# Kernel optimization log

Hardware: AMD Instinct MI355X
Metric: run time of the kernel (lower is better)

## Reference

```python
import jax, jax.numpy as jnp
import numpy as np

N, E, T = 20000, 320000, 4
F_IN, HID, F_OUT = 128, 256, 128
EPS = 1e-5  # torch BatchNorm1d default


def _gcn_layer(x, src, dst, ew, W, b, gamma, beta):
    # gather-scale-scatter: out[dst] += ew_e * x[src]
    msgs = ew[:, :, None] * x[src]                      # (E, T, F)
    agg = jax.ops.segment_sum(msgs, dst, num_segments=N)  # (N, T, F)
    h = jnp.einsum('ntf,fh->nth', agg, W) + b            # (N, T, H)
    # BatchNorm1d over channel dim H (training-mode batch stats over N and T)
    mean = h.mean(axis=(0, 1))
    var = h.var(axis=(0, 1))
    h = (h - mean) * jax.lax.rsqrt(var + EPS) * gamma + beta
    return jax.nn.relu(h)


def setup_inputs() -> dict:
    key = jax.random.key(0)
    ks = jax.random.split(key, 8)
    node_features = jax.random.normal(ks[0], (N, T, F_IN), jnp.float32)
    edge_index = jax.random.randint(ks[1], (2, E), 0, N, dtype=jnp.int32)
    edges_weight = jax.random.uniform(ks[2], (E, T), jnp.float32)
    s0 = 1.0 / np.sqrt(F_IN)
    s1 = 1.0 / np.sqrt(HID)
    W0 = jax.random.uniform(ks[3], (F_IN, HID), jnp.float32, -s0, s0)
    b0 = jax.random.uniform(ks[4], (HID,), jnp.float32, -s0, s0)
    W1 = jax.random.uniform(ks[5], (HID, F_OUT), jnp.float32, -s1, s1)
    b1 = jax.random.uniform(ks[6], (F_OUT,), jnp.float32, -s1, s1)
    g0 = jnp.ones((HID,), jnp.float32)
    be0 = jnp.zeros((HID,), jnp.float32)
    g1 = jnp.ones((F_OUT,), jnp.float32)
    be1 = jnp.zeros((F_OUT,), jnp.float32)
    return {"node_features": node_features, "edge_index": edge_index,
            "edges_weight": edges_weight, "W0": W0, "b0": b0, "g0": g0,
            "be0": be0, "W1": W1, "b1": b1, "g1": g1, "be1": be1}


def reference(node_features, edge_index, edges_weight,
              W0, b0, g0, be0, W1, b1, g1, be1):
    src, dst = edge_index[0], edge_index[1]
    h = _gcn_layer(node_features, src, dst, edges_weight, W0, b0, g0, be0)
    h = _gcn_layer(h, src, dst, edges_weight, W1, b1, g1, be1)
    return h
```

## Files before the change

### kernel.cpp

```cpp
#include <hip/hip_runtime.h>


#define T_DIM 4
#define F_DIM 128
#define HID   256
#define TF    512

__global__ void count_kernel(const int* __restrict__ dst, int E, int* __restrict__ deg) {
    int e = blockIdx.x * blockDim.x + threadIdx.x;
    if (e < E) atomicAdd(&deg[dst[e]], 1);
}

__global__ void scan_kernel(const int* __restrict__ deg, int* __restrict__ row_start,
                            int* __restrict__ cursor, int n) {
    __shared__ int part[1024];
    int tid = threadIdx.x;
    int chunk = (n + 1023) >> 10;
    int begin = tid * chunk;
    if (begin > n) begin = n;
    int end = begin + chunk;
    if (end > n) end = n;
    int s = 0;
    for (int i = begin; i < end; ++i) s += deg[i];
    part[tid] = s;
    __syncthreads();
    for (int off = 1; off < 1024; off <<= 1) {
        int v = (tid >= off) ? part[tid - off] : 0;
        __syncthreads();
        part[tid] += v;
        __syncthreads();
    }
    int excl = (tid == 0) ? 0 : part[tid - 1];
    for (int i = begin; i < end; ++i) {
        row_start[i] = excl;
        cursor[i] = excl;
        excl += deg[i];
    }
    if (tid == 1023) row_start[n] = part[1023];
}

__global__ void fill_kernel(const int* __restrict__ src, const int* __restrict__ dst,
                            const float4* __restrict__ ew, int E,
                            int* __restrict__ cursor, int* __restrict__ esrc,
                            float4* __restrict__ ewr) {
    int e = blockIdx.x * blockDim.x + threadIdx.x;
    if (e < E) {
        int d = dst[e];
        int p = atomicAdd(&cursor[d], 1);
        esrc[p] = src[e];
        ewr[p] = ew[e];
    }
}

__global__ __launch_bounds__(256) void agg_kernel(
        const float* __restrict__ x, const float* __restrict__ ewr,
        const int* __restrict__ row_start, const int* __restrict__ esrc,
        float* __restrict__ out) {
    const int n = blockIdx.x;
    const int j = threadIdx.x;
    const int t0 = j >> 7;
    const int beg = row_start[n], end = row_start[n + 1];
    float acc0 = 0.f, acc1 = 0.f;
    for (int i = beg; i < end; ++i) {
        const int s = esrc[i];
        const float* xr = x + (size_t)s * TF;
        const float w0 = ewr[i * T_DIM + t0];
        const float w1 = ewr[i * T_DIM + t0 + 2];
        acc0 = fmaf(w0, xr[j], acc0);
        acc1 = fmaf(w1, xr[j + 256], acc1);
    }
    const size_t o = (size_t)n * TF + j;
    out[o] = acc0;
    out[o + 256] = acc1;
}

template<int K, int NC, bool FUSE>
__global__ __launch_bounds__(256, 4) void gemm_kernel(
        const float* __restrict__ A, const float* __restrict__ W,
        const float* __restrict__ scale, const float* __restrict__ shift,
        float* __restrict__ out) {
    constexpr int BM = 128, BN = 128, BK = 32;
    constexpr int ASTR = BK + 4;
    __shared__ float Al[BM * ASTR];
    __shared__ float Wl[BK * BN];
    const int tid = threadIdx.x;
    const long rowbase = (long)blockIdx.y * BM;
    const int colbase = blockIdx.x * BN;
    const int trow = tid >> 4;
    const int tcol = tid & 15;

    float acc[8][8] = {};

    const int nk = K / BK;
    for (int kb = 0; kb < nk; ++kb) {
        #pragma unroll
        for (int it = 0; it < 4; ++it) {
            int idx = tid + it * 256;
            int r = idx >> 3, q = idx & 7;
            float4 v = *(const float4*)&A[(rowbase + r) * K + kb * BK + q * 4];
            if (FUSE) {
                int ch = kb * BK + q * 4;
                float4 sc = *(const float4*)&scale[ch];
                float4 sh = *(const float4*)&shift[ch];
                v.x = fmaxf(fmaf(sc.x, v.x, sh.x), 0.f);
                v.y = fmaxf(fmaf(sc.y, v.y, sh.y), 0.f);
                v.z = fmaxf(fmaf(sc.z, v.z, sh.z), 0.f);
                v.w = fmaxf(fmaf(sc.w, v.w, sh.w), 0.f);
            }
            *(float4*)&Al[r * ASTR + q * 4] = v;
        }
        #pragma unroll
        for (int it = 0; it < 4; ++it) {
            int idx = tid + it * 256;
            int k = idx >> 5, c4 = idx & 31;
            *(float4*)&Wl[k * BN + c4 * 4] =
                *(const float4*)&W[(long)(kb * BK + k) * NC + colbase + c4 * 4];
        }
        __syncthreads();

        #pragma unroll
        for (int kk = 0; kk < BK; ++kk) {
            float a[8], w[8];
            #pragma unroll
            for (int i = 0; i < 8; ++i) a[i] = Al[(trow + 16 * i) * ASTR + kk];
            *(float4*)&w[0] = *(const float4*)&Wl[kk * BN + tcol * 8];
            *(float4*)&w[4] = *(const float4*)&Wl[kk * BN + tcol * 8 + 4];
            #pragma unroll
            for (int i = 0; i < 8; ++i)
                #pragma unroll
                for (int j = 0; j < 8; ++j)
                    acc[i][j] = fmaf(a[i], w[j], acc[i][j]);
        }
        __syncthreads();
    }

    #pragma unroll
    for (int i = 0; i < 8; ++i) {
        float* op = &out[(rowbase + trow + 16 * i) * NC + colbase + tcol * 8];
        *(float4*)&op[0] = make_float4(acc[i][0], acc[i][1], acc[i][2], acc[i][3]);
        *(float4*)&op[4] = make_float4(acc[i][4], acc[i][5], acc[i][6], acc[i][7]);
    }
}

template<int C>
__global__ __launch_bounds__(256) void stats_kernel(
        const float* __restrict__ h, int rows,
        float* __restrict__ sums, float* __restrict__ sqs) {
    constexpr int Q = C / 4;
    constexpr int RPB = 256 / Q;
    const int q = threadIdx.x & (Q - 1);
    const int sub = threadIdx.x / Q;
    float4 s = make_float4(0.f, 0.f, 0.f, 0.f);
    float4 s2 = make_float4(0.f, 0.f, 0.f, 0.f);
    for (long r = (long)blockIdx.x * RPB + sub; r < rows; r += (long)gridDim.x * RPB) {
        float4 v = *(const float4*)&h[r * C + q * 4];
        s.x += v.x; s.y += v.y; s.z += v.z; s.w += v.w;
        s2.x = fmaf(v.x, v.x, s2.x); s2.y = fmaf(v.y, v.y, s2.y);
        s2.z = fmaf(v.z, v.z, s2.z); s2.w = fmaf(v.w, v.w, s2.w);
    }
    __shared__ float4 redS[256], redQ[256];
    redS[threadIdx.x] = s;
    redQ[threadIdx.x] = s2;
    __syncthreads();
    if (sub == 0) {
        #pragma unroll
        for (int u = 1; u < RPB; ++u) {
            float4 a = redS[u * Q + q], b = redQ[u * Q + q];
            s.x += a.x; s.y += a.y; s.z += a.z; s.w += a.w;
            s2.x += b.x; s2.y += b.y; s2.z += b.z; s2.w += b.w;
        }
        atomicAdd(&sums[q * 4 + 0], s.x);
        atomicAdd(&sums[q * 4 + 1], s.y);
        atomicAdd(&sums[q * 4 + 2], s.z);
        atomicAdd(&sums[q * 4 + 3], s.w);
        atomicAdd(&sqs[q * 4 + 0], s2.x);
        atomicAdd(&sqs[q * 4 + 1], s2.y);
        atomicAdd(&sqs[q * 4 + 2], s2.z);
        atomicAdd(&sqs[q * 4 + 3], s2.w);
    }
}

__global__ void finalize_kernel(const float* __restrict__ sums, const float* __restrict__ sqs,
                                const float* __restrict__ g, const float* __restrict__ be,
                                float* __restrict__ scale, float* __restrict__ shift,
                                int C, float invR) {
    int c = threadIdx.x;
    if (c < C) {
        float mean = sums[c] * invR;
        float var = sqs[c] * invR - mean * mean;
        float a = g[c] * rsqrtf(var + 1e-5f);
        scale[c] = a;
        shift[c] = fmaf(-mean, a, be[c]);
    }
}

__global__ void bnapply_kernel(const float4* __restrict__ h4,
                               const float* __restrict__ scale, const float* __restrict__ shift,
                               float4* __restrict__ out4, int n4) {
    int i = blockIdx.x * 256 + threadIdx.x;
    if (i >= n4) return;
    float4 v = h4[i];
    int cb = (i & 31) << 2;
    float4 sc = *(const float4*)&scale[cb];
    float4 sh = *(const float4*)&shift[cb];
    v.x = fmaxf(fmaf(sc.x, v.x, sh.x), 0.f);
    v.y = fmaxf(fmaf(sc.y, v.y, sh.y), 0.f);
    v.z = fmaxf(fmaf(sc.z, v.z, sh.z), 0.f);
    v.w = fmaxf(fmaf(sc.w, v.w, sh.w), 0.f);
    out4[i] = v;
}

extern "C" void kernel_launch(void* const* d_in, const int* in_sizes, int n_in,
                              void* d_out, int out_size, void* d_ws, size_t ws_size,
                              hipStream_t stream) {
    const float* x   = (const float*)d_in[0];
    const int*   ei  = (const int*)d_in[1];
    const float* ew  = (const float*)d_in[2];
    const float* W0  = (const float*)d_in[3];
    const float* g0  = (const float*)d_in[5];
    const float* be0 = (const float*)d_in[6];
    const float* W1  = (const float*)d_in[7];
    const float* g1  = (const float*)d_in[9];
    const float* be1 = (const float*)d_in[10];
    float* out = (float*)d_out;

    const int N = in_sizes[0] / TF;
    const int E = in_sizes[1] / 2;
    const int ROWS = N * T_DIM;

    const int* src = ei;
    const int* dst = ei + E;

    float* h1   = (float*)d_ws;
    float* bufC = h1 + (size_t)ROWS * HID;
    float* h2   = bufC + (size_t)ROWS * F_DIM;
    int* deg       = (int*)(h2 + (size_t)ROWS * F_DIM);
    int* row_start = deg + N;
    int* cursor    = row_start + N + 1;
    int* esrc      = cursor + N + 1;
    float* ewr     = (float*)(esrc + E);
    float* sums0   = ewr + (size_t)E * 4;
    float* sqs0    = sums0 + HID;
    float* sums1   = sqs0 + HID;
    float* sqs1    = sums1 + F_DIM;
    float* scale0  = sqs1 + F_DIM;
    float* shift0  = scale0 + HID;
    float* scale1  = shift0 + HID;
    float* shift1  = scale1 + F_DIM;

    hipMemsetAsync(deg, 0, N * sizeof(int), stream);
    hipMemsetAsync(sums0, 0, (2 * HID + 2 * F_DIM) * sizeof(float), stream);

    const int eb = (E + 255) / 256;
    count_kernel<<<eb, 256, 0, stream>>>(dst, E, deg);
    scan_kernel<<<1, 1024, 0, stream>>>(deg, row_start, cursor, N);
    fill_kernel<<<eb, 256, 0, stream>>>(src, dst, (const float4*)ew, E, cursor,
                                        esrc, (float4*)ewr);

    agg_kernel<<<N, 256, 0, stream>>>(x, ewr, row_start, esrc, bufC);
    gemm_kernel<128, 256, false><<<dim3(2, ROWS / 128), 256, 0, stream>>>(
        bufC, W0, nullptr, nullptr, h1);
    stats_kernel<256><<<256, 256, 0, stream>>>(h1, ROWS, sums0, sqs0);
    finalize_kernel<<<1, 256, 0, stream>>>(sums0, sqs0, g0, be0, scale0, shift0, HID,
                                           1.f / (float)ROWS);

    gemm_kernel<256, 128, true><<<dim3(1, ROWS / 128), 256, 0, stream>>>(
        h1, W1, scale0, shift0, bufC);
    agg_kernel<<<N, 256, 0, stream>>>(bufC, ewr, row_start, esrc, h2);
    stats_kernel<128><<<256, 256, 0, stream>>>(h2, ROWS, sums1, sqs1);
    finalize_kernel<<<1, 128, 0, stream>>>(sums1, sqs1, g1, be1, scale1, shift1, F_DIM,
                                           1.f / (float)ROWS);
    bnapply_kernel<<<(ROWS * F_DIM / 4 + 255) / 256, 256, 0, stream>>>(
        (const float4*)h2, scale1, shift1, (float4*)out, ROWS * F_DIM / 4);
}
```

Before: 651.3 us.

## Split aggregation edges across thread groups and vectorize GEMM shared-memory reads

The aggregation kernel now has four 64-thread groups, each handling every fourth edge with float4 loads of 8 features per thread. The per-group partial sums are then reduced through shared memory, so more gather loads are in flight per node. The GEMM reads A as float4 across four k-steps and uses a strided column mapping for W reads and output stores, which is meant to cut shared-memory bank conflicts. The second GEMM uses a 64-row tile to launch more blocks. The trade-offs are the extra shared-memory reduction and sync in aggregation, and idle groups on low-degree nodes.

Measured after the change: 614.2 us. 1.06x faster.

```diff
diff --git a/kernel.cpp b/kernel.cpp
--- a/kernel.cpp
+++ b/kernel.cpp
@@ -53,33 +53,52 @@
 }
 
 __global__ __launch_bounds__(256) void agg_kernel(
-        const float* __restrict__ x, const float* __restrict__ ewr,
+        const float4* __restrict__ x4, const float* __restrict__ ewr,
         const int* __restrict__ row_start, const int* __restrict__ esrc,
-        float* __restrict__ out) {
+        float4* __restrict__ out4) {
     const int n = blockIdx.x;
-    const int j = threadIdx.x;
-    const int t0 = j >> 7;
+    const int tid = threadIdx.x;
+    const int p = tid >> 6;
+    const int q = tid & 63;
+    const int t = q >> 4;
     const int beg = row_start[n], end = row_start[n + 1];
-    float acc0 = 0.f, acc1 = 0.f;
-    for (int i = beg; i < end; ++i) {
-        const int s = esrc[i];
-        const float* xr = x + (size_t)s * TF;
-        const float w0 = ewr[i * T_DIM + t0];
-        const float w1 = ewr[i * T_DIM + t0 + 2];
-        acc0 = fmaf(w0, xr[j], acc0);
-        acc1 = fmaf(w1, xr[j + 256], acc1);
-    }
-    const size_t o = (size_t)n * TF + j;
-    out[o] = acc0;
-    out[o + 256] = acc1;
-}
-
-template<int K, int NC, bool FUSE>
+    float4 accA = make_float4(0.f, 0.f, 0.f, 0.f);
+    float4 accB = make_float4(0.f, 0.f, 0.f, 0.f);
+    for (int i = beg; i < end; i += 4) {
+        const int e = i + p;
+        if (e < end) {
+            const int s = esrc[e];
+            const float4* xr = x4 + (size_t)s * 128;
+            const float w = ewr[e * 4 + t];
+            float4 va = xr[2 * q], vb = xr[2 * q + 1];
+            accA.x = fmaf(w, va.x, accA.x); accA.y = fmaf(w, va.y, accA.y);
+            accA.z = fmaf(w, va.z, accA.z); accA.w = fmaf(w, va.w, accA.w);
+            accB.x = fmaf(w, vb.x, accB.x); accB.y = fmaf(w, vb.y, accB.y);
+            accB.z = fmaf(w, vb.z, accB.z); accB.w = fmaf(w, vb.w, accB.w);
+        }
+    }
+    __shared__ float4 red[3][128];
+    if (p) { red[p - 1][2 * q] = accA; red[p - 1][2 * q + 1] = accB; }
+    __syncthreads();
+    if (p == 0) {
+        #pragma unroll
+        for (int r = 0; r < 3; ++r) {
+            float4 a = red[r][2 * q], b = red[r][2 * q + 1];
+            accA.x += a.x; accA.y += a.y; accA.z += a.z; accA.w += a.w;
+            accB.x += b.x; accB.y += b.y; accB.z += b.z; accB.w += b.w;
+        }
+        out4[(size_t)n * 128 + 2 * q] = accA;
+        out4[(size_t)n * 128 + 2 * q + 1] = accB;
+    }
+}
+
+template<int BM, int K, int NC, bool FUSE>
 __global__ __launch_bounds__(256, 4) void gemm_kernel(
         const float* __restrict__ A, const float* __restrict__ W,
         const float* __restrict__ scale, const float* __restrict__ shift,
         float* __restrict__ out) {
-    constexpr int BM = 128, BN = 128, BK = 32;
+    constexpr int BN = 128, BK = 32;
+    constexpr int RPT = BM / 16;
     constexpr int ASTR = BK + 4;
     __shared__ float Al[BM * ASTR];
     __shared__ float Wl[BK * BN];
@@ -89,12 +108,12 @@
     const int trow = tid >> 4;
     const int tcol = tid & 15;
 
-    float acc[8][8] = {};
+    float acc[RPT][8] = {};
 
     const int nk = K / BK;
     for (int kb = 0; kb < nk; ++kb) {
         #pragma unroll
-        for (int it = 0; it < 4; ++it) {
+        for (int it = 0; it < BM * BK / 1024; ++it) {
             int idx = tid + it * 256;
             int r = idx >> 3, q = idx & 7;
             float4 v = *(const float4*)&A[(rowbase + r) * K + kb * BK + q * 4];
@@ -119,26 +138,35 @@
         __syncthreads();
 
         #pragma unroll
-        for (int kk = 0; kk < BK; ++kk) {
-            float a[8], w[8];
+        for (int kk4 = 0; kk4 < BK / 4; ++kk4) {
+            float4 a4[RPT];
             #pragma unroll
-            for (int i = 0; i < 8; ++i) a[i] = Al[(trow + 16 * i) * ASTR + kk];
-            *(float4*)&w[0] = *(const float4*)&Wl[kk * BN + tcol * 8];
-            *(float4*)&w[4] = *(const float4*)&Wl[kk * BN + tcol * 8 + 4];
+            for (int i = 0; i < RPT; ++i)
+                a4[i] = *(const float4*)&Al[(trow + 16 * i) * ASTR + kk4 * 4];
             #pragma unroll
-            for (int i = 0; i < 8; ++i)
+            for (int q = 0; q < 4; ++q) {
+                const int kk = kk4 * 4 + q;
+                float w[8];
+                *(float4*)&w[0] = *(const float4*)&Wl[kk * BN + tcol * 4];
+                *(float4*)&w[4] = *(const float4*)&Wl[kk * BN + 64 + tcol * 4];
                 #pragma unroll
-                for (int j = 0; j < 8; ++j)
-                    acc[i][j] = fmaf(a[i], w[j], acc[i][j]);
+                for (int i = 0; i < RPT; ++i) {
+                    const float a = (q == 0) ? a4[i].x : (q == 1) ? a4[i].y
+                                  : (q == 2) ? a4[i].z : a4[i].w;
+                    #pragma unroll
+                    for (int j = 0; j < 8; ++j)
+                        acc[i][j] = fmaf(a, w[j], acc[i][j]);
+                }
+            }
         }
         __syncthreads();
     }
 
     #pragma unroll
-    for (int i = 0; i < 8; ++i) {
-        float* op = &out[(rowbase + trow + 16 * i) * NC + colbase + tcol * 8];
-        *(float4*)&op[0] = make_float4(acc[i][0], acc[i][1], acc[i][2], acc[i][3]);
-        *(float4*)&op[4] = make_float4(acc[i][4], acc[i][5], acc[i][6], acc[i][7]);
+    for (int i = 0; i < RPT; ++i) {
+        float* op = &out[(rowbase + trow + 16 * i) * NC + colbase + tcol * 4];
+        *(float4*)&op[0]  = make_float4(acc[i][0], acc[i][1], acc[i][2], acc[i][3]);
+        *(float4*)&op[64] = make_float4(acc[i][4], acc[i][5], acc[i][6], acc[i][7]);
     }
 }
 
@@ -257,16 +285,18 @@
     fill_kernel<<<eb, 256, 0, stream>>>(src, dst, (const float4*)ew, E, cursor,
                                         esrc, (float4*)ewr);
 
-    agg_kernel<<<N, 256, 0, stream>>>(x, ewr, row_start, esrc, bufC);
-    gemm_kernel<128, 256, false><<<dim3(2, ROWS / 128), 256, 0, stream>>>(
+    agg_kernel<<<N, 256, 0, stream>>>((const float4*)x, ewr, row_start, esrc,
+                                      (float4*)bufC);
+    gemm_kernel<128, 128, 256, false><<<dim3(2, ROWS / 128), 256, 0, stream>>>(
         bufC, W0, nullptr, nullptr, h1);
     stats_kernel<256><<<256, 256, 0, stream>>>(h1, ROWS, sums0, sqs0);
     finalize_kernel<<<1, 256, 0, stream>>>(sums0, sqs0, g0, be0, scale0, shift0, HID,
                                            1.f / (float)ROWS);
 
-    gemm_kernel<256, 128, true><<<dim3(1, ROWS / 128), 256, 0, stream>>>(
+    gemm_kernel<64, 256, 128, true><<<dim3(1, ROWS / 64), 256, 0, stream>>>(
         h1, W1, scale0, shift0, bufC);
-    agg_kernel<<<N, 256, 0, stream>>>(bufC, ewr, row_start, esrc, h2);
+    agg_kernel<<<N, 256, 0, stream>>>((const float4*)bufC, ewr, row_start, esrc,
+                                      (float4*)h2);
     stats_kernel<128><<<256, 256, 0, stream>>>(h2, ROWS, sums1, sqs1);
     finalize_kernel<<<1, 128, 0, stream>>>(sums1, sqs1, g1, be1, scale1, shift1, F_DIM,
                                            1.f / (float)ROWS);
```
